# Kernel optimization log

Hardware: AMD Instinct MI355X
Metric: run time of the kernel (lower is better)

Reference implementation:

```python
import jax, jax.numpy as jnp
import numpy as np

LORA_SCALING = 16.0 / 8.0  # lora_alpha / lora_r


def setup_inputs() -> dict:
    key = jax.random.key(0)
    k_x, k_m, k_wm, k_bm, k_wa, k_wb = jax.random.split(key, 6)
    B, S, D_in, D_out, R = 4, 2048, 4096, 4096, 8
    x = jax.random.normal(k_x, (B, S, D_in), dtype=jnp.float32)
    im_mask = jax.random.randint(k_m, (B, S), 0, 2) > 0  # bool token mask
    # Linear weights stored torch-style: [out, in]
    W_main = jax.random.normal(k_wm, (D_out, D_in), dtype=jnp.float32) * (1.0 / np.sqrt(D_in))
    b_main = jax.random.normal(k_bm, (D_out,), dtype=jnp.float32) * 0.01
    W_A = jax.random.normal(k_wa, (R, D_in), dtype=jnp.float32) * (1.0 / np.sqrt(D_in))
    W_B = jax.random.normal(k_wb, (D_out, R), dtype=jnp.float32) * (1.0 / np.sqrt(R))
    return {"x": x, "im_mask": im_mask, "W_main": W_main, "b_main": b_main, "W_A": W_A, "W_B": W_B}


def reference(x, im_mask, W_main, b_main, W_A, W_B):
    # Main dense path: res = x @ W_main.T + b
    res = jnp.einsum('bsd,od->bso', x, W_main) + b_main
    # LoRA path applied only at masked tokens (dropout disabled / eval):
    # res[im_mask] += (x[im_mask] @ W_A.T) @ W_B.T * scaling
    # Static-shape equivalent: compute everywhere, mask the add.
    lora = jnp.einsum('bsr,or->bso', jnp.einsum('bsd,rd->bsr', x, W_A), W_B)
    return res + jnp.where(im_mask[..., None], lora * LORA_SCALING, jnp.zeros((), x.dtype))
```

## Files before the change

kernel.cpp:

```cpp
#include <hip/hip_runtime.h>

typedef unsigned short u16;
typedef unsigned int   u32;
typedef unsigned long long u64;
typedef __bf16 bf16x8 __attribute__((ext_vector_type(8)));
typedef float  f32x4  __attribute__((ext_vector_type(4)));

#define AS1 __attribute__((address_space(1)))
#define AS3 __attribute__((address_space(3)))

#define M_TOK 8192
#define K_DIM 4096
#define N_DIM 4096
#define BK    32
#define NKT   (K_DIM / BK)

static __device__ __forceinline__ u16 f2bf(float f) {
  u32 u = __builtin_bit_cast(u32, f);
  return (u16)((u + (0x7FFFu + ((u >> 16) & 1u))) >> 16);
}

static __device__ __forceinline__ void gld_lds16(const void* g, void* l) {
  __builtin_amdgcn_global_load_lds((AS1 u32*)(u64)g, (AS3 u32*)(u32)(u64)l, 16, 0, 0);
}

__global__ __launch_bounds__(256) void k_prep(const float* __restrict__ x,
                                              const float* __restrict__ WA,
                                              const float* __restrict__ W,
                                              u16* __restrict__ xb,
                                              float* __restrict__ mid,
                                              u16* __restrict__ Wb) {
  const int t = threadIdx.x;
  if (blockIdx.x >= M_TOK) {
    const int cb = blockIdx.x - M_TOK;
    const float4* W4 = (const float4*)W;
    ushort4* Wb4 = (ushort4*)Wb;
    const int n4 = (N_DIM * K_DIM) / 4;
    int i = cb * 256 + t;
    for (; i < n4; i += 2048 * 256) {
      float4 v = W4[i];
      ushort4 o;
      o.x = f2bf(v.x); o.y = f2bf(v.y); o.z = f2bf(v.z); o.w = f2bf(v.w);
      Wb4[i] = o;
    }
    return;
  }
  const int m = blockIdx.x;
  const float4* xr = (const float4*)(x + (size_t)m * K_DIM);
  ushort4* xbr = (ushort4*)(xb + (size_t)m * K_DIM);
  float a[8] = {0.f,0.f,0.f,0.f,0.f,0.f,0.f,0.f};
  #pragma unroll
  for (int i = 0; i < 4; ++i) {
    const int k4 = t + i * 256;
    float4 v = xr[k4];
    ushort4 o;
    o.x = f2bf(v.x); o.y = f2bf(v.y); o.z = f2bf(v.z); o.w = f2bf(v.w);
    xbr[k4] = o;
    #pragma unroll
    for (int r = 0; r < 8; ++r) {
      float4 wv = ((const float4*)(WA + (size_t)r * K_DIM))[k4];
      a[r] += v.x * wv.x + v.y * wv.y + v.z * wv.z + v.w * wv.w;
    }
  }
  #pragma unroll
  for (int r = 0; r < 8; ++r) {
    #pragma unroll
    for (int off = 32; off > 0; off >>= 1)
      a[r] += __shfl_down(a[r], off);
  }
  __shared__ float red[4][8];
  const int w = t >> 6, l = t & 63;
  if (l == 0) {
    #pragma unroll
    for (int r = 0; r < 8; ++r) red[w][r] = a[r];
  }
  __syncthreads();
  if (t < 8)
    mid[(size_t)m * 8 + t] = 2.0f * (red[0][t] + red[1][t] + red[2][t] + red[3][t]);
}

__global__ __launch_bounds__(512, 2) void k_gemm(
    const u16* __restrict__ A, const u16* __restrict__ B,
    const float* __restrict__ bias, const int* __restrict__ mask,
    const float* __restrict__ mid, const float* __restrict__ WBw,
    float* __restrict__ out) {
  __shared__ u16 smem[2][2][256][BK];

  const int t = threadIdx.x;
  const int wid = t >> 6, l = t & 63;
  const int wr = wid >> 2, wc = wid & 3;
  const int fr = l & 15, fq = l >> 4;

  const int bid = blockIdx.x;
  const int swz = (bid & 7) * 64 + (bid >> 3);
  const int bm = swz >> 4, bn = swz & 15;

  const char* Ag = (const char*)(A + (size_t)bm * 256 * K_DIM);
  const char* Bg = (const char*)(B + (size_t)bn * 256 * K_DIM);
  const size_t rowb = (size_t)K_DIM * 2;

  const int srow = t >> 2;
  const int schk = (((t & 3) ^ ((t >> 3) & 3)) * 16);
  const char* gA0 = Ag + (size_t)srow * rowb + schk;
  const char* gA1 = Ag + (size_t)(128 + srow) * rowb + schk;
  const char* gB0 = Bg + (size_t)srow * rowb + schk;
  const char* gB1 = Bg + (size_t)(128 + srow) * rowb + schk;
  char* lbase = (char*)&smem[0][0][0][0] + wid * 1024;

  f32x4 acc[8][4];
  #pragma unroll
  for (int m = 0; m < 8; ++m)
    #pragma unroll
    for (int n = 0; n < 4; ++n)
      acc[m][n] = (f32x4){0.f, 0.f, 0.f, 0.f};

  gld_lds16(gA0, lbase);
  gld_lds16(gA1, lbase + 8192);
  gld_lds16(gB0, lbase + 16384);
  gld_lds16(gB1, lbase + 24576);
  asm volatile("s_waitcnt vmcnt(0)" ::: "memory");
  __builtin_amdgcn_s_barrier();

  const int csw = (fq ^ ((fr >> 1) & 3)) * 8;

  #define K_TILE(BUFC, NB, DOSTAGE, GOFF, DOWAIT) do {                       \
    if (DOSTAGE) {                                                           \
      gld_lds16(gA0 + (GOFF), lbase + (NB) * 32768);                         \
      gld_lds16(gA1 + (GOFF), lbase + (NB) * 32768 + 8192);                  \
      gld_lds16(gB0 + (GOFF), lbase + (NB) * 32768 + 16384);                 \
      gld_lds16(gB1 + (GOFF), lbase + (NB) * 32768 + 24576);                 \
    }                                                                        \
    {                                                                        \
      const u16* Ab_ = &smem[BUFC][0][wr * 128 + fr][csw];                   \
      const u16* Bb_ = &smem[BUFC][1][wc * 64 + fr][csw];                    \
      bf16x8 af_[8], bf_[4];                                                 \
      _Pragma("unroll")                                                      \
      for (int m = 0; m < 8; ++m)                                            \
        af_[m] = *(const bf16x8*)(Ab_ + m * 16 * BK);                        \
      _Pragma("unroll")                                                      \
      for (int n = 0; n < 4; ++n)                                            \
        bf_[n] = *(const bf16x8*)(Bb_ + n * 16 * BK);                        \
      __builtin_amdgcn_s_setprio(1);                                         \
      _Pragma("unroll")                                                      \
      for (int m = 0; m < 8; ++m)                                            \
        _Pragma("unroll")                                                    \
        for (int n = 0; n < 4; ++n)                                          \
          acc[m][n] = __builtin_amdgcn_mfma_f32_16x16x32_bf16(               \
              af_[m], bf_[n], acc[m][n], 0, 0, 0);                           \
      __builtin_amdgcn_s_setprio(0);                                         \
    }                                                                        \
    if (DOWAIT) {                                                            \
      asm volatile("s_waitcnt vmcnt(0)" ::: "memory");                       \
      __builtin_amdgcn_s_barrier();                                          \
    }                                                                        \
  } while (0)

  for (int ktb = 0; ktb < NKT - 2; ktb += 2) {
    K_TILE(0, 1, true, 64,  true);
    K_TILE(1, 0, true, 128, true);
    gA0 += 128; gA1 += 128; gB0 += 128; gB1 += 128;
  }
  K_TILE(0, 1, true,  64, true);
  K_TILE(1, 0, false, 0,  false);

  #undef K_TILE

  const int gn0 = bn * 256 + wc * 64;
  const size_t gm0 = (size_t)bm * 256 + wr * 128;
  float wbv[4][8]; float bv[4];
  #pragma unroll
  for (int n = 0; n < 4; ++n) {
    const int gn = gn0 + n * 16 + fr;
    bv[n] = bias[gn];
    const float4 w0 = ((const float4*)(WBw + (size_t)gn * 8))[0];
    const float4 w1 = ((const float4*)(WBw + (size_t)gn * 8))[1];
    wbv[n][0] = w0.x; wbv[n][1] = w0.y; wbv[n][2] = w0.z; wbv[n][3] = w0.w;
    wbv[n][4] = w1.x; wbv[n][5] = w1.y; wbv[n][6] = w1.z; wbv[n][7] = w1.w;
  }
  #pragma unroll
  for (int m = 0; m < 8; ++m) {
    #pragma unroll
    for (int j = 0; j < 4; ++j) {
      const size_t gm = gm0 + m * 16 + fq * 4 + j;
      const int msk = mask[gm];
      const float4 m0 = ((const float4*)(mid + gm * 8))[0];
      const float4 m1 = ((const float4*)(mid + gm * 8))[1];
      float* orow = out + gm * (size_t)N_DIM;
      #pragma unroll
      for (int n = 0; n < 4; ++n) {
        const float lora =
            m0.x * wbv[n][0] + m0.y * wbv[n][1] + m0.z * wbv[n][2] + m0.w * wbv[n][3] +
            m1.x * wbv[n][4] + m1.y * wbv[n][5] + m1.z * wbv[n][6] + m1.w * wbv[n][7];
        orow[gn0 + n * 16 + fr] = acc[m][n][j] + bv[n] + (msk ? lora : 0.0f);
      }
    }
  }
}

extern "C" void kernel_launch(void* const* d_in, const int* in_sizes, int n_in,
                              void* d_out, int out_size, void* d_ws, size_t ws_size,
                              hipStream_t stream) {
  (void)in_sizes; (void)n_in; (void)out_size; (void)ws_size;
  const float* x     = (const float*)d_in[0];
  const int*   mask  = (const int*)d_in[1];
  const float* Wm    = (const float*)d_in[2];
  const float* bmain = (const float*)d_in[3];
  const float* WA    = (const float*)d_in[4];
  const float* WB    = (const float*)d_in[5];
  float* out = (float*)d_out;

  u16* xb  = (u16*)d_ws;
  u16* wb  = xb + (size_t)M_TOK * K_DIM;
  float* mid = (float*)(wb + (size_t)N_DIM * K_DIM);

  k_prep<<<M_TOK + 2048, 256, 0, stream>>>(x, WA, Wm, xb, mid, wb);
  dim3 grid((M_TOK / 256) * (N_DIM / 256));
  k_gemm<<<grid, 512, 0, stream>>>(xb, wb, bmain, mask, mid, WB, out);
}
```

Before: 349.2 us.

## Double K tile to 64 and split each tile into four barrier-synced phases

After: 322.0 us (median of 2 runs). -7.8%, faster.

```diff
diff --git a/kernel.cpp b/kernel.cpp
--- a/kernel.cpp
+++ b/kernel.cpp
@@ -12,7 +12,7 @@
 #define M_TOK 8192
 #define K_DIM 4096
 #define N_DIM 4096
-#define BK    32
+#define BK    64
 #define NKT   (K_DIM / BK)
 
 static __device__ __forceinline__ u16 f2bf(float f) {
@@ -84,7 +84,8 @@
     const float* __restrict__ bias, const int* __restrict__ mask,
     const float* __restrict__ mid, const float* __restrict__ WBw,
     float* __restrict__ out) {
-  __shared__ u16 smem[2][2][256][BK];
+  __shared__ u16 smem[2][2][256][64];
+  char* lds = (char*)&smem[0][0][0][0];
 
   const int t = threadIdx.x;
   const int wid = t >> 6, l = t & 63;
@@ -99,13 +100,22 @@
   const char* Bg = (const char*)(B + (size_t)bn * 256 * K_DIM);
   const size_t rowb = (size_t)K_DIM * 2;
 
-  const int srow = t >> 2;
-  const int schk = (((t & 3) ^ ((t >> 3) & 3)) * 16);
-  const char* gA0 = Ag + (size_t)srow * rowb + schk;
-  const char* gA1 = Ag + (size_t)(128 + srow) * rowb + schk;
-  const char* gB0 = Bg + (size_t)srow * rowb + schk;
-  const char* gB1 = Bg + (size_t)(128 + srow) * rowb + schk;
-  char* lbase = (char*)&smem[0][0][0][0] + wid * 1024;
+  const int srow8 = t >> 3;
+  const int schk = (((t & 7) ^ ((t >> 3) & 7)) * 16);
+  const char* sA0 = Ag + (size_t)(  0 + srow8) * rowb + schk;
+  const char* sA1 = Ag + (size_t)( 64 + srow8) * rowb + schk;
+  const char* sA2 = Ag + (size_t)(128 + srow8) * rowb + schk;
+  const char* sA3 = Ag + (size_t)(192 + srow8) * rowb + schk;
+  const char* sB0 = Bg + (size_t)(  0 + srow8) * rowb + schk;
+  const char* sB1 = Bg + (size_t)( 64 + srow8) * rowb + schk;
+  const char* sB2 = Bg + (size_t)(128 + srow8) * rowb + schk;
+  const char* sB3 = Bg + (size_t)(192 + srow8) * rowb + schk;
+  const int widoff = wid * 1024;
+
+  const int so0 = ((fq) ^ (fr & 7)) * 16;
+  const int so1 = ((4 + fq) ^ (fr & 7)) * 16;
+  const int aoff = (wr * 128 + fr) * 128;
+  const int boff = 32768 + (wc * 64 + fr) * 128;
 
   f32x4 acc[8][4];
   #pragma unroll
@@ -114,56 +124,82 @@
     for (int n = 0; n < 4; ++n)
       acc[m][n] = (f32x4){0.f, 0.f, 0.f, 0.f};
 
-  gld_lds16(gA0, lbase);
-  gld_lds16(gA1, lbase + 8192);
-  gld_lds16(gB0, lbase + 16384);
-  gld_lds16(gB1, lbase + 24576);
+  gld_lds16(sB0, lds + 32768 +     0 + widoff);
+  gld_lds16(sB1, lds + 32768 +  8192 + widoff);
+  gld_lds16(sB2, lds + 32768 + 16384 + widoff);
+  gld_lds16(sB3, lds + 32768 + 24576 + widoff);
+  gld_lds16(sA0, lds +     0 + widoff);
+  gld_lds16(sA2, lds + 16384 + widoff);
+  gld_lds16(sA1, lds +  8192 + widoff);
+  gld_lds16(sA3, lds + 24576 + widoff);
   asm volatile("s_waitcnt vmcnt(0)" ::: "memory");
   __builtin_amdgcn_s_barrier();
 
-  const int csw = (fq ^ ((fr >> 1) & 3)) * 8;
-
-  #define K_TILE(BUFC, NB, DOSTAGE, GOFF, DOWAIT) do {                       \
+  bf16x8 bq[8];
+
+  #define VM4 asm volatile("s_waitcnt vmcnt(4)" ::: "memory")
+  #define VM2 asm volatile("s_waitcnt vmcnt(2)" ::: "memory")
+  #define VM0 asm volatile("s_waitcnt vmcnt(0)" ::: "memory")
+  #define NOW ((void)0)
+
+  #define PHASE(BUF, Q, LOADB, DOSTAGE, S0, S1, D0, D1, GOFF, WAIT) do {     \
+    const char* Ab_ = lds + (BUF) * 65536 + aoff;                            \
+    bf16x8 a0_ = *(const bf16x8*)(Ab_ + (2*(Q)) * 2048 + so0);               \
+    bf16x8 a1_ = *(const bf16x8*)(Ab_ + (2*(Q)) * 2048 + so1);               \
+    bf16x8 a2_ = *(const bf16x8*)(Ab_ + (2*(Q)+1) * 2048 + so0);             \
+    bf16x8 a3_ = *(const bf16x8*)(Ab_ + (2*(Q)+1) * 2048 + so1);             \
+    if (LOADB) {                                                             \
+      const char* Bb_ = lds + (BUF) * 65536 + boff;                          \
+      _Pragma("unroll")                                                      \
+      for (int n = 0; n < 4; ++n) {                                          \
+        bq[2*n]   = *(const bf16x8*)(Bb_ + n * 2048 + so0);                  \
+        bq[2*n+1] = *(const bf16x8*)(Bb_ + n * 2048 + so1);                  \
+      }                                                                      \
+    }                                                                        \
     if (DOSTAGE) {                                                           \
-      gld_lds16(gA0 + (GOFF), lbase + (NB) * 32768);                         \
-      gld_lds16(gA1 + (GOFF), lbase + (NB) * 32768 + 8192);                  \
-      gld_lds16(gB0 + (GOFF), lbase + (NB) * 32768 + 16384);                 \
-      gld_lds16(gB1 + (GOFF), lbase + (NB) * 32768 + 24576);                 \
+      gld_lds16((S0) + (GOFF), lds + ((BUF)^1) * 65536 + (D0) + widoff);     \
+      gld_lds16((S1) + (GOFF), lds + ((BUF)^1) * 65536 + (D1) + widoff);     \
     }                                                                        \
-    {                                                                        \
-      const u16* Ab_ = &smem[BUFC][0][wr * 128 + fr][csw];                   \
-      const u16* Bb_ = &smem[BUFC][1][wc * 64 + fr][csw];                    \
-      bf16x8 af_[8], bf_[4];                                                 \
-      _Pragma("unroll")                                                      \
-      for (int m = 0; m < 8; ++m)                                            \
-        af_[m] = *(const bf16x8*)(Ab_ + m * 16 * BK);                        \
-      _Pragma("unroll")                                                      \
-      for (int n = 0; n < 4; ++n)                                            \
-        bf_[n] = *(const bf16x8*)(Bb_ + n * 16 * BK);                        \
-      __builtin_amdgcn_s_setprio(1);                                         \
-      _Pragma("unroll")                                                      \
-      for (int m = 0; m < 8; ++m)                                            \
-        _Pragma("unroll")                                                    \
-        for (int n = 0; n < 4; ++n)                                          \
-          acc[m][n] = __builtin_amdgcn_mfma_f32_16x16x32_bf16(               \
-              af_[m], bf_[n], acc[m][n], 0, 0, 0);                           \
-      __builtin_amdgcn_s_setprio(0);                                         \
+    __builtin_amdgcn_sched_barrier(0);                                       \
+    __builtin_amdgcn_s_barrier();                                            \
+    __builtin_amdgcn_s_setprio(1);                                           \
+    _Pragma("unroll")                                                        \
+    for (int n = 0; n < 4; ++n) {                                            \
+      acc[2*(Q)][n]   = __builtin_amdgcn_mfma_f32_16x16x32_bf16(             \
+          a0_, bq[2*n],   acc[2*(Q)][n],   0, 0, 0);                         \
+      acc[2*(Q)][n]   = __builtin_amdgcn_mfma_f32_16x16x32_bf16(             \
+          a1_, bq[2*n+1], acc[2*(Q)][n],   0, 0, 0);                         \
+      acc[2*(Q)+1][n] = __builtin_amdgcn_mfma_f32_16x16x32_bf16(             \
+          a2_, bq[2*n],   acc[2*(Q)+1][n], 0, 0, 0);                         \
+      acc[2*(Q)+1][n] = __builtin_amdgcn_mfma_f32_16x16x32_bf16(             \
+          a3_, bq[2*n+1], acc[2*(Q)+1][n], 0, 0, 0);                         \
     }                                                                        \
-    if (DOWAIT) {                                                            \
-      asm volatile("s_waitcnt vmcnt(0)" ::: "memory");                       \
-      __builtin_amdgcn_s_barrier();                                          \
-    }                                                                        \
+    __builtin_amdgcn_s_setprio(0);                                           \
+    WAIT;                                                                    \
+    __builtin_amdgcn_s_barrier();                                            \
   } while (0)
 
-  for (int ktb = 0; ktb < NKT - 2; ktb += 2) {
-    K_TILE(0, 1, true, 64,  true);
-    K_TILE(1, 0, true, 128, true);
-    gA0 += 128; gA1 += 128; gB0 += 128; gB1 += 128;
-  }
-  K_TILE(0, 1, true,  64, true);
-  K_TILE(1, 0, false, 0,  false);
+  #define K_TILE(BUF, DOSTAGE, GOFF, W1, W3)                                 \
+    PHASE(BUF, 0, true,  DOSTAGE, sB0, sB1, 32768+0,     32768+8192,  GOFF, NOW); \
+    PHASE(BUF, 1, false, DOSTAGE, sB2, sB3, 32768+16384, 32768+24576, GOFF, W1);  \
+    PHASE(BUF, 2, false, DOSTAGE, sA0, sA2, 0,           16384,       GOFF, NOW); \
+    PHASE(BUF, 3, false, DOSTAGE, sA1, sA3, 8192,        24576,       GOFF, W3)
+
+  for (int it = 0; it < 31; ++it) {
+    K_TILE(0, true, 128, VM4, VM2);
+    K_TILE(1, true, 256, VM4, VM2);
+    sA0 += 256; sA1 += 256; sA2 += 256; sA3 += 256;
+    sB0 += 256; sB1 += 256; sB2 += 256; sB3 += 256;
+  }
+  K_TILE(0, true, 128, VM4, VM2);
+  K_TILE(1, false, 0, VM0, NOW);
 
   #undef K_TILE
+  #undef PHASE
+  #undef VM4
+  #undef VM2
+  #undef VM0
+  #undef NOW
 
   const int gn0 = bn * 256 + wc * 64;
   const size_t gm0 = (size_t)bm * 256 + wr * 128;
```

## Use 1024-thread GEMM blocks with a 4-stage LDS pipeline

Applied to the files above, without the earlier changes.

New measurement: 344.3 us. No clear change (-1.4%).

```diff
diff --git a/kernel.cpp b/kernel.cpp
--- a/kernel.cpp
+++ b/kernel.cpp
@@ -79,12 +79,12 @@
     mid[(size_t)m * 8 + t] = 2.0f * (red[0][t] + red[1][t] + red[2][t] + red[3][t]);
 }
 
-__global__ __launch_bounds__(512, 2) void k_gemm(
+__global__ __launch_bounds__(1024) void k_gemm(
     const u16* __restrict__ A, const u16* __restrict__ B,
     const float* __restrict__ bias, const int* __restrict__ mask,
     const float* __restrict__ mid, const float* __restrict__ WBw,
     float* __restrict__ out) {
-  __shared__ u16 smem[2][2][256][BK];
+  __shared__ u16 smem[4][2][256][BK];
 
   const int t = threadIdx.x;
   const int wid = t >> 6, l = t & 63;
@@ -101,72 +101,83 @@
 
   const int srow = t >> 2;
   const int schk = (((t & 3) ^ ((t >> 3) & 3)) * 16);
-  const char* gA0 = Ag + (size_t)srow * rowb + schk;
-  const char* gA1 = Ag + (size_t)(128 + srow) * rowb + schk;
-  const char* gB0 = Bg + (size_t)srow * rowb + schk;
-  const char* gB1 = Bg + (size_t)(128 + srow) * rowb + schk;
+  const char* gA = Ag + (size_t)srow * rowb + schk;
+  const char* gB = Bg + (size_t)srow * rowb + schk;
   char* lbase = (char*)&smem[0][0][0][0] + wid * 1024;
 
-  f32x4 acc[8][4];
-  #pragma unroll
-  for (int m = 0; m < 8; ++m)
+  f32x4 acc[4][4];
+  #pragma unroll
+  for (int m = 0; m < 4; ++m)
     #pragma unroll
     for (int n = 0; n < 4; ++n)
       acc[m][n] = (f32x4){0.f, 0.f, 0.f, 0.f};
 
-  gld_lds16(gA0, lbase);
-  gld_lds16(gA1, lbase + 8192);
-  gld_lds16(gB0, lbase + 16384);
-  gld_lds16(gB1, lbase + 24576);
-  asm volatile("s_waitcnt vmcnt(0)" ::: "memory");
+  #pragma unroll
+  for (int pk = 0; pk < 3; ++pk) {
+    gld_lds16(gA + pk * 64, lbase + pk * 32768);
+    gld_lds16(gB + pk * 64, lbase + pk * 32768 + 16384);
+  }
+  asm volatile("s_waitcnt vmcnt(4)" ::: "memory");
   __builtin_amdgcn_s_barrier();
 
   const int csw = (fq ^ ((fr >> 1) & 3)) * 8;
 
-  #define K_TILE(BUFC, NB, DOSTAGE, GOFF, DOWAIT) do {                       \
+  const char* pA = gA + 192;
+  const char* pB = gB + 192;
+
+  #define K_TILE(BUFC, NB, DOSTAGE, GOFF, WAIT) do {                         \
     if (DOSTAGE) {                                                           \
-      gld_lds16(gA0 + (GOFF), lbase + (NB) * 32768);                         \
-      gld_lds16(gA1 + (GOFF), lbase + (NB) * 32768 + 8192);                  \
-      gld_lds16(gB0 + (GOFF), lbase + (NB) * 32768 + 16384);                 \
-      gld_lds16(gB1 + (GOFF), lbase + (NB) * 32768 + 24576);                 \
+      gld_lds16(pA + (GOFF), lbase + (NB) * 32768);                          \
+      gld_lds16(pB + (GOFF), lbase + (NB) * 32768 + 16384);                  \
     }                                                                        \
     {                                                                        \
-      const u16* Ab_ = &smem[BUFC][0][wr * 128 + fr][csw];                   \
+      const u16* Ab_ = &smem[BUFC][0][wr * 64 + fr][csw];                    \
       const u16* Bb_ = &smem[BUFC][1][wc * 64 + fr][csw];                    \
-      bf16x8 af_[8], bf_[4];                                                 \
+      bf16x8 af_[4], bf_[4];                                                 \
       _Pragma("unroll")                                                      \
-      for (int m = 0; m < 8; ++m)                                            \
+      for (int m = 0; m < 4; ++m)                                            \
         af_[m] = *(const bf16x8*)(Ab_ + m * 16 * BK);                        \
       _Pragma("unroll")                                                      \
       for (int n = 0; n < 4; ++n)                                            \
         bf_[n] = *(const bf16x8*)(Bb_ + n * 16 * BK);                        \
       __builtin_amdgcn_s_setprio(1);                                         \
       _Pragma("unroll")                                                      \
-      for (int m = 0; m < 8; ++m)                                            \
+      for (int m = 0; m < 4; ++m)                                            \
         _Pragma("unroll")                                                    \
         for (int n = 0; n < 4; ++n)                                          \
           acc[m][n] = __builtin_amdgcn_mfma_f32_16x16x32_bf16(               \
               af_[m], bf_[n], acc[m][n], 0, 0, 0);                           \
       __builtin_amdgcn_s_setprio(0);                                         \
     }                                                                        \
-    if (DOWAIT) {                                                            \
-      asm volatile("s_waitcnt vmcnt(0)" ::: "memory");                       \
-      __builtin_amdgcn_s_barrier();                                          \
-    }                                                                        \
+    WAIT;                                                                    \
+    __builtin_amdgcn_s_barrier();                                            \
   } while (0)
 
-  for (int ktb = 0; ktb < NKT - 2; ktb += 2) {
-    K_TILE(0, 1, true, 64,  true);
-    K_TILE(1, 0, true, 128, true);
-    gA0 += 128; gA1 += 128; gB0 += 128; gB1 += 128;
-  }
-  K_TILE(0, 1, true,  64, true);
-  K_TILE(1, 0, false, 0,  false);
+  #define VM4 asm volatile("s_waitcnt vmcnt(4)" ::: "memory")
+  #define VM2 asm volatile("s_waitcnt vmcnt(2)" ::: "memory")
+  #define VM0 asm volatile("s_waitcnt vmcnt(0)" ::: "memory")
+  #define NOW ((void)0)
+
+  for (int ktb = 0; ktb < NKT - 4; ktb += 4) {
+    K_TILE(0, 3, true, 0,   VM4);
+    K_TILE(1, 0, true, 64,  VM4);
+    K_TILE(2, 1, true, 128, VM4);
+    K_TILE(3, 2, true, 192, VM4);
+    pA += 256; pB += 256;
+  }
+  K_TILE(0, 3, true,  0, VM4);
+  K_TILE(1, 0, false, 0, VM2);
+  K_TILE(2, 1, false, 0, VM0);
+  K_TILE(3, 2, false, 0, NOW);
 
   #undef K_TILE
+  #undef VM4
+  #undef VM2
+  #undef VM0
+  #undef NOW
 
   const int gn0 = bn * 256 + wc * 64;
-  const size_t gm0 = (size_t)bm * 256 + wr * 128;
+  const size_t gm0 = (size_t)bm * 256 + wr * 64;
   float wbv[4][8]; float bv[4];
   #pragma unroll
   for (int n = 0; n < 4; ++n) {
@@ -178,7 +189,7 @@
     wbv[n][4] = w1.x; wbv[n][5] = w1.y; wbv[n][6] = w1.z; wbv[n][7] = w1.w;
   }
   #pragma unroll
-  for (int m = 0; m < 8; ++m) {
+  for (int m = 0; m < 4; ++m) {
     #pragma unroll
     for (int j = 0; j < 4; ++j) {
       const size_t gm = gm0 + m * 16 + fq * 4 + j;
@@ -215,5 +226,5 @@
 
   k_prep<<<M_TOK + 2048, 256, 0, stream>>>(x, WA, Wm, xb, mid, wb);
   dim3 grid((M_TOK / 256) * (N_DIM / 256));
-  k_gemm<<<grid, 512, 0, stream>>>(xb, wb, bmain, mask, mid, WB, out);
-}
+  k_gemm<<<grid, 1024, 0, stream>>>(xb, wb, bmain, mask, mid, WB, out);
+}
```

## Shrink GEMM tile to 256x128 with 4 waves and triple-buffered LDS pipeline

Applied to the files above, without the earlier changes.

Result: slower. 359.8 us (+3.0%).

```diff
diff --git a/kernel.cpp b/kernel.cpp
--- a/kernel.cpp
+++ b/kernel.cpp
@@ -79,33 +79,36 @@
     mid[(size_t)m * 8 + t] = 2.0f * (red[0][t] + red[1][t] + red[2][t] + red[3][t]);
 }
 
-__global__ __launch_bounds__(512, 2) void k_gemm(
+__global__ __launch_bounds__(256, 2) void k_gemm(
     const u16* __restrict__ A, const u16* __restrict__ B,
     const float* __restrict__ bias, const int* __restrict__ mask,
     const float* __restrict__ mid, const float* __restrict__ WBw,
     float* __restrict__ out) {
-  __shared__ u16 smem[2][2][256][BK];
+  __shared__ u16 smem[3][12288];
+  char* lds = (char*)&smem[0][0];
 
   const int t = threadIdx.x;
   const int wid = t >> 6, l = t & 63;
-  const int wr = wid >> 2, wc = wid & 3;
+  const int wr = wid >> 1, wc = wid & 1;
   const int fr = l & 15, fq = l >> 4;
 
   const int bid = blockIdx.x;
-  const int swz = (bid & 7) * 64 + (bid >> 3);
-  const int bm = swz >> 4, bn = swz & 15;
+  const int swz = (bid & 7) * 128 + (bid >> 3);
+  const int bm = swz >> 5, bn = swz & 31;
 
   const char* Ag = (const char*)(A + (size_t)bm * 256 * K_DIM);
-  const char* Bg = (const char*)(B + (size_t)bn * 256 * K_DIM);
+  const char* Bg = (const char*)(B + (size_t)bn * 128 * K_DIM);
   const size_t rowb = (size_t)K_DIM * 2;
 
   const int srow = t >> 2;
   const int schk = (((t & 3) ^ ((t >> 3) & 3)) * 16);
-  const char* gA0 = Ag + (size_t)srow * rowb + schk;
-  const char* gA1 = Ag + (size_t)(128 + srow) * rowb + schk;
-  const char* gB0 = Bg + (size_t)srow * rowb + schk;
-  const char* gB1 = Bg + (size_t)(128 + srow) * rowb + schk;
-  char* lbase = (char*)&smem[0][0][0][0] + wid * 1024;
+  const char* sA0 = Ag + (size_t)(  0 + srow) * rowb + schk;
+  const char* sA1 = Ag + (size_t)( 64 + srow) * rowb + schk;
+  const char* sA2 = Ag + (size_t)(128 + srow) * rowb + schk;
+  const char* sA3 = Ag + (size_t)(192 + srow) * rowb + schk;
+  const char* sB0 = Bg + (size_t)(  0 + srow) * rowb + schk;
+  const char* sB1 = Bg + (size_t)( 64 + srow) * rowb + schk;
+  const int widoff = wid * 1024;
 
   f32x4 acc[8][4];
   #pragma unroll
@@ -114,32 +117,54 @@
     for (int n = 0; n < 4; ++n)
       acc[m][n] = (f32x4){0.f, 0.f, 0.f, 0.f};
 
-  gld_lds16(gA0, lbase);
-  gld_lds16(gA1, lbase + 8192);
-  gld_lds16(gB0, lbase + 16384);
-  gld_lds16(gB1, lbase + 24576);
-  asm volatile("s_waitcnt vmcnt(0)" ::: "memory");
+  #define STAGE6(BUFV, GOFF) do {                                            \
+    char* b_ = lds + (BUFV) * 24576 + widoff;                                \
+    gld_lds16(sA0 + (GOFF), b_);                                             \
+    gld_lds16(sA1 + (GOFF), b_ + 4096);                                      \
+    gld_lds16(sA2 + (GOFF), b_ + 8192);                                      \
+    gld_lds16(sA3 + (GOFF), b_ + 12288);                                     \
+    gld_lds16(sB0 + (GOFF), b_ + 16384);                                     \
+    gld_lds16(sB1 + (GOFF), b_ + 20480);                                     \
+  } while (0)
+
+  STAGE6(0, 0);
+  STAGE6(1, 64);
+  asm volatile("s_waitcnt vmcnt(6)" ::: "memory");
   __builtin_amdgcn_s_barrier();
 
   const int csw = (fq ^ ((fr >> 1) & 3)) * 8;
 
-  #define K_TILE(BUFC, NB, DOSTAGE, GOFF, DOWAIT) do {                       \
-    if (DOSTAGE) {                                                           \
-      gld_lds16(gA0 + (GOFF), lbase + (NB) * 32768);                         \
-      gld_lds16(gA1 + (GOFF), lbase + (NB) * 32768 + 8192);                  \
-      gld_lds16(gB0 + (GOFF), lbase + (NB) * 32768 + 16384);                 \
-      gld_lds16(gB1 + (GOFF), lbase + (NB) * 32768 + 24576);                 \
-    }                                                                        \
+  const char* base = (const char*)0;
+  (void)base;
+  #define ADV(P) P += 192
+  const char* pA0 = sA0 + 128; const char* pA1 = sA1 + 128;
+  const char* pA2 = sA2 + 128; const char* pA3 = sA3 + 128;
+  const char* pB0 = sB0 + 128; const char* pB1 = sB1 + 128;
+
+  #define STAGE6P(BUFV, GOFF) do {                                           \
+    char* b_ = lds + (BUFV) * 24576 + widoff;                                \
+    gld_lds16(pA0 + (GOFF), b_);                                             \
+    gld_lds16(pA1 + (GOFF), b_ + 4096);                                      \
+    gld_lds16(pA2 + (GOFF), b_ + 8192);                                      \
+    gld_lds16(pA3 + (GOFF), b_ + 12288);                                     \
+    gld_lds16(pB0 + (GOFF), b_ + 16384);                                     \
+    gld_lds16(pB1 + (GOFF), b_ + 20480);                                     \
+  } while (0)
+
+  #define K_TILE(BUFC, NB, DOSTAGE, GOFF, WAIT) do {                         \
+    if (DOSTAGE) STAGE6P(NB, GOFF);                                          \
     {                                                                        \
-      const u16* Ab_ = &smem[BUFC][0][wr * 128 + fr][csw];                   \
-      const u16* Bb_ = &smem[BUFC][1][wc * 64 + fr][csw];                    \
+      const u16* Ab_ = (const u16*)(lds + (BUFC) * 24576)                    \
+                       + (wr * 128 + fr) * 32 + csw;                         \
+      const u16* Bb_ = (const u16*)(lds + (BUFC) * 24576 + 16384)            \
+                       + (wc * 64 + fr) * 32 + csw;                          \
       bf16x8 af_[8], bf_[4];                                                 \
       _Pragma("unroll")                                                      \
       for (int m = 0; m < 8; ++m)                                            \
-        af_[m] = *(const bf16x8*)(Ab_ + m * 16 * BK);                        \
+        af_[m] = *(const bf16x8*)(Ab_ + m * 16 * 32);                        \
       _Pragma("unroll")                                                      \
       for (int n = 0; n < 4; ++n)                                            \
-        bf_[n] = *(const bf16x8*)(Bb_ + n * 16 * BK);                        \
+        bf_[n] = *(const bf16x8*)(Bb_ + n * 16 * 32);                        \
       __builtin_amdgcn_s_setprio(1);                                         \
       _Pragma("unroll")                                                      \
       for (int m = 0; m < 8; ++m)                                            \
@@ -149,23 +174,32 @@
               af_[m], bf_[n], acc[m][n], 0, 0, 0);                           \
       __builtin_amdgcn_s_setprio(0);                                         \
     }                                                                        \
-    if (DOWAIT) {                                                            \
-      asm volatile("s_waitcnt vmcnt(0)" ::: "memory");                       \
-      __builtin_amdgcn_s_barrier();                                          \
-    }                                                                        \
+    WAIT;                                                                    \
+    __builtin_amdgcn_s_barrier();                                            \
   } while (0)
 
-  for (int ktb = 0; ktb < NKT - 2; ktb += 2) {
-    K_TILE(0, 1, true, 64,  true);
-    K_TILE(1, 0, true, 128, true);
-    gA0 += 128; gA1 += 128; gB0 += 128; gB1 += 128;
-  }
-  K_TILE(0, 1, true,  64, true);
-  K_TILE(1, 0, false, 0,  false);
+  #define VM6 asm volatile("s_waitcnt vmcnt(6)" ::: "memory")
+  #define VM0 asm volatile("s_waitcnt vmcnt(0)" ::: "memory")
+  #define NOW ((void)0)
+
+  for (int g = 0; g < 42; ++g) {
+    K_TILE(0, 2, true, 0,   VM6);
+    K_TILE(1, 0, true, 64,  VM6);
+    K_TILE(2, 1, true, 128, VM6);
+    ADV(pA0); ADV(pA1); ADV(pA2); ADV(pA3); ADV(pB0); ADV(pB1);
+  }
+  K_TILE(0, 2, false, 0, VM0);
+  K_TILE(1, 0, false, 0, NOW);
 
   #undef K_TILE
-
-  const int gn0 = bn * 256 + wc * 64;
+  #undef STAGE6P
+  #undef STAGE6
+  #undef ADV
+  #undef VM6
+  #undef VM0
+  #undef NOW
+
+  const int gn0 = bn * 128 + wc * 64;
   const size_t gm0 = (size_t)bm * 256 + wr * 128;
   float wbv[4][8]; float bv[4];
   #pragma unroll
@@ -214,6 +248,6 @@
   float* mid = (float*)(wb + (size_t)N_DIM * K_DIM);
 
   k_prep<<<M_TOK + 2048, 256, 0, stream>>>(x, WA, Wm, xb, mid, wb);
-  dim3 grid((M_TOK / 256) * (N_DIM / 256));
-  k_gemm<<<grid, 512, 0, stream>>>(xb, wb, bmain, mask, mid, WB, out);
-}
+  dim3 grid((M_TOK / 256) * (N_DIM / 128));
+  k_gemm<<<grid, 256, 0, stream>>>(xb, wb, bmain, mask, mid, WB, out);
+}
```
